# Optimization experiments

Measured on AMD Instinct MI355X. Metric: run time of the kernel, lower is better.

Reference implementation:

```python
import jax, jax.numpy as jnp
import numpy as np

N_NODES = 100000
N_EDGES = 1600000
N_FEAT = 128
N_HID = 128
N_CLS = 40
DROP_P = 0.5


def setup_inputs() -> dict:
    key = jax.random.key(0)
    k1, k2, k3, k4 = jax.random.split(key, 4)
    x = jax.random.normal(k1, (N_NODES, N_FEAT), dtype=jnp.float32)
    edge_index = jax.random.randint(k2, (2, N_EDGES), 0, N_NODES, dtype=jnp.int32)
    W1 = jax.random.normal(k3, (N_FEAT, N_HID), dtype=jnp.float32) / np.sqrt(N_FEAT)
    b1 = jnp.zeros((N_HID,), dtype=jnp.float32)
    W2 = jax.random.normal(k4, (N_HID, N_CLS), dtype=jnp.float32) / np.sqrt(N_HID)
    b2 = jnp.zeros((N_CLS,), dtype=jnp.float32)
    return {"x": x, "edge_index": edge_index, "W1": W1, "b1": b1, "W2": W2, "b2": b2}


def _gcn_norm(edge_index, num_nodes):
    # add self-loops, then symmetric normalization D^-1/2 (A+I) D^-1/2
    loops = jnp.arange(num_nodes, dtype=edge_index.dtype)
    src = jnp.concatenate([edge_index[0], loops])
    dst = jnp.concatenate([edge_index[1], loops])
    deg = jax.ops.segment_sum(jnp.ones_like(dst, dtype=jnp.float32), dst,
                              num_segments=num_nodes)
    deg_isqrt = jax.lax.rsqrt(deg)  # deg >= 1 thanks to self-loops
    norm = deg_isqrt[src] * deg_isqrt[dst]  # [E+N]
    return src, dst, norm


def _gcn_conv(x, src, dst, norm, W, b, num_nodes):
    h = x @ W                                   # [N, out]
    msg = h[src] * norm[:, None]                # gather + scale, [E+N, out]
    out = jax.ops.segment_sum(msg, dst, num_segments=num_nodes)  # scatter-add
    return out + b


def reference(x, edge_index, W1, b1, W2, b2):
    num_nodes = x.shape[0]
    src, dst, norm = _gcn_norm(edge_index, num_nodes)
    h = _gcn_conv(x, src, dst, norm, W1, b1, num_nodes)
    h = jax.nn.relu(h)
    # dropout(p=0.5, training=True) with a fixed key for determinism
    keep = jax.random.uniform(jax.random.key(42), h.shape) >= DROP_P
    h = jnp.where(keep, h / (1.0 - DROP_P), 0.0)
    out = _gcn_conv(h, src, dst, norm, W2, b2, num_nodes)
    return out
```

## Files before the change

kernel.cpp:

```cpp
#include <hip/hip_runtime.h>

#define N_NODES 100000
#define N_EDGES 1600000
#define NBUCK 196
#define G1B 1563
#define FB 391
#define FEDGE 4096
#define BCAP 9216

typedef __attribute__((ext_vector_type(8))) short short8v;
typedef __attribute__((ext_vector_type(4))) float f32x4;

__device__ __forceinline__ unsigned pack_bf16(float a, float b){
  unsigned ua = __float_as_uint(a), ub = __float_as_uint(b);
  ua = ua + 0x7fffu + ((ua >> 16) & 1u);
  ub = ub + 0x7fffu + ((ub >> 16) & 1u);
  return (ua >> 16) | (ub & 0xffff0000u);
}
__device__ __forceinline__ unsigned short bf16_of(float a){
  unsigned ua = __float_as_uint(a);
  ua = ua + 0x7fffu + ((ua >> 16) & 1u);
  return (unsigned short)(ua >> 16);
}
__device__ __forceinline__ float bf_lo(unsigned u){ return __uint_as_float(u << 16); }
__device__ __forceinline__ float bf_hi(unsigned u){ return __uint_as_float(u & 0xffff0000u); }

__device__ __forceinline__ unsigned tf_rotl(unsigned x, int r){ return (x<<r)|(x>>(32-r)); }

__device__ __forceinline__ unsigned dropout_keep(unsigned e){
  unsigned x0 = 0u, x1 = e;
  const unsigned k0 = 0u, k1v = 42u;
  const unsigned k2 = 0x1BD11BDAu ^ k0 ^ k1v;
#define TF_R(r) { x0 += x1; x1 = tf_rotl(x1,(r)); x1 ^= x0; }
  x0 += k0; x1 += k1v;
  TF_R(13) TF_R(15) TF_R(26) TF_R(6)
  x0 += k1v; x1 += k2 + 1u;
  TF_R(17) TF_R(29) TF_R(16) TF_R(24)
  x0 += k2; x1 += k0 + 2u;
  TF_R(13) TF_R(15) TF_R(26) TF_R(6)
  x0 += k0; x1 += k1v + 3u;
  TF_R(17) TF_R(29) TF_R(16) TF_R(24)
  x0 += k1v; x1 += k2 + 4u;
  TF_R(13) TF_R(15) TF_R(26) TF_R(6)
  x0 += k2; x1 += k0 + 5u;
#undef TF_R
  return (x0 ^ x1) >> 31;
}

__global__ void k_init(const float* __restrict__ W1, const float* __restrict__ W2,
                       unsigned short* __restrict__ W1T, unsigned short* __restrict__ W2T48,
                       int* __restrict__ bcur2){
  int b = blockIdx.x, t = threadIdx.x;
  if (b < 64){
    int idx = b*256 + t;
    int k = idx >> 7, n = idx & 127;
    W1T[n*128 + k] = bf16_of(W1[idx]);
  } else {
    if (t < NBUCK) bcur2[t] = 0;
    for (int i = t; i < 48*128; i += 256){
      int c = i >> 7, k = i & 127;
      W2T48[c*128 + k] = (c < 40) ? bf16_of(W2[k*40 + c]) : (unsigned short)0;
    }
  }
}

__launch_bounds__(256)
__global__ void k_B(const float* __restrict__ x, const unsigned short* __restrict__ W1T,
                    unsigned short* __restrict__ h1u,
                    const int* __restrict__ src, const int* __restrict__ dst,
                    int* __restrict__ bcur2, unsigned* __restrict__ tmp, int N, int E){
  __shared__ int hist[4][200];
  int t = threadIdx.x;
  if (blockIdx.x < FB){
    int fb = blockIdx.x;
    int w = t >> 6, lane = t & 63;
    for (int i = lane; i < NBUCK; i += 64) hist[w][i] = 0;
    __syncthreads();
    int e0 = fb*FEDGE;
    #pragma unroll 4
    for (int j = 0; j < FEDGE/256; j++){
      int e = e0 + t + j*256;
      if (e < E) atomicAdd(&hist[w][dst[e] >> 9], 1);
    }
    __syncthreads();
    if (t < NBUCK){
      int c0 = hist[0][t], c1 = hist[1][t], c2 = hist[2][t], c3 = hist[3][t];
      int tot = c0 + c1 + c2 + c3;
      int base = 0;
      if (tot > 0) base = t*BCAP + atomicAdd(&bcur2[t], tot);
      hist[0][t] = base;
      hist[1][t] = base + c0;
      hist[2][t] = base + c0 + c1;
      hist[3][t] = base + c0 + c1 + c2;
    }
    __syncthreads();
    #pragma unroll 4
    for (int j = 0; j < FEDGE/256; j++){
      int e = e0 + t + j*256;
      if (e < E){
        int d = dst[e], s = src[e];
        int p = atomicAdd(&hist[w][d >> 9], 1);
        tmp[p] = ((unsigned)(d & 511) << 17) | (unsigned)s;
      }
    }
    return;
  }
  int gb = blockIdx.x - FB;
  if (gb >= G1B) return;
  int w = t >> 6, l = t & 63;
  int lo = l & 15, hi = l >> 4;
  int rowA = gb*64 + w*16 + lo;
  int rA = (rowA < N) ? rowA : (N-1);
  const float4* xr = (const float4*)(x + (size_t)rA*128);

  short8v a[4];
  #pragma unroll
  for (int kk = 0; kk < 4; kk++){
    float4 f0 = xr[kk*8 + 2*hi];
    float4 f1 = xr[kk*8 + 2*hi + 1];
    union { short8v v; unsigned u[4]; } A;
    A.u[0] = pack_bf16(f0.x, f0.y);
    A.u[1] = pack_bf16(f0.z, f0.w);
    A.u[2] = pack_bf16(f1.x, f1.y);
    A.u[3] = pack_bf16(f1.z, f1.w);
    a[kk] = A.v;
  }
  int rowC0 = gb*64 + w*16 + hi*4;
  #pragma unroll
  for (int tt = 0; tt < 8; tt++){
    int n0 = tt*16;
    const uint4* brow = (const uint4*)(W1T + (n0 + lo)*128);
    f32x4 acc = {0.f, 0.f, 0.f, 0.f};
    #pragma unroll
    for (int kk = 0; kk < 4; kk++){
      union { short8v v; uint4 q; } B;
      B.q = brow[kk*4 + hi];
      acc = __builtin_amdgcn_mfma_f32_16x16x32_bf16(a[kk], B.v, acc, 0, 0, 0);
    }
    int colC = n0 + lo;
    #pragma unroll
    for (int r = 0; r < 4; r++){
      int rc = rowC0 + r;
      if (rc < N) h1u[(size_t)rc*128 + colC] = bf16_of(acc[r]);
    }
  }
}

__launch_bounds__(1024)
__global__ void k_hist(const unsigned* __restrict__ tmp, const int* __restrict__ bcur2,
                       int* __restrict__ degi, int* __restrict__ off,
                       float* __restrict__ dii, int N){
  __shared__ int cur[512];
  __shared__ int wtot[8];
  int b = blockIdx.x, t = threadIdx.x;
  if (t < 512) cur[t] = 0;
  __syncthreads();
  int m = bcur2[b];
  int base = b*BCAP;
  int node0 = b << 9;
  for (int i = t; i < m; i += 1024)
    atomicAdd(&cur[tmp[base + i] >> 17], 1);
  __syncthreads();
  if (t < 512){
    int v = cur[t];
    int lane = t & 63, w = t >> 6;
    int incl = v;
    for (int d = 1; d < 64; d <<= 1){
      int y = __shfl_up(incl, d);
      if (lane >= d) incl += y;
    }
    if (lane == 63) wtot[w] = incl;
    __syncthreads();
    int wb = 0;
    for (int i = 0; i < w; i++) wb += wtot[i];
    int excl = wb + incl - v;
    int n = node0 + t;
    if (n < N){
      degi[n] = v;
      off[n]  = base + excl;
      dii[n]  = rsqrtf((float)(v + 1));
    }
  }
}

__launch_bounds__(1024)
__global__ void k_csort(const unsigned* __restrict__ tmp, int2* __restrict__ csre,
                        const int* __restrict__ off, const int* __restrict__ bcur2,
                        const float* __restrict__ dii, int N){
  __shared__ int   cur[512];
  __shared__ float dl[512];
  int b = blockIdx.x, t = threadIdx.x;
  int node0 = b << 9;
  if (t < 512){
    int n = node0 + t;
    cur[t] = (n < N) ? off[n] : 0;
    dl[t]  = (n < N) ? dii[n] : 0.f;
  }
  __syncthreads();
  int m = bcur2[b];
  int base = b*BCAP;
  for (int i = t; i < m; i += 1024){
    unsigned e = tmp[base + i];
    int dloc = e >> 17;
    int s = e & 0x1FFFFu;
    float w = dii[s] * dl[dloc];
    int p = atomicAdd(&cur[dloc], 1);
    csre[p] = make_int2(s, __float_as_int(w));
  }
}

__launch_bounds__(256)
__global__ void k_agg1(const unsigned* __restrict__ h1g, unsigned* __restrict__ Bbg,
                       const int2* __restrict__ csre, const int* __restrict__ off,
                       const int* __restrict__ degi, const float* __restrict__ dii,
                       const float* __restrict__ b1, int N){
  int n = blockIdx.x*4 + (threadIdx.x >> 6);
  int lane = threadIdx.x & 63;
  if (n >= N) return;
  n = __builtin_amdgcn_readfirstlane(n);
  float din = dii[n];
  float s2 = din*din;
  unsigned su = h1g[(size_t)n*64 + lane];
  float a0 = bf_lo(su)*s2, a1 = bf_hi(su)*s2;
  int o = off[n], cnt = degi[n];
  int i = 0;
  for (; i + 8 <= cnt; i += 8){
    int2 e0 = csre[o+i+0], e1 = csre[o+i+1], e2 = csre[o+i+2], e3 = csre[o+i+3];
    int2 e4 = csre[o+i+4], e5 = csre[o+i+5], e6 = csre[o+i+6], e7 = csre[o+i+7];
    unsigned u0 = h1g[(size_t)e0.x*64 + lane];
    unsigned u1 = h1g[(size_t)e1.x*64 + lane];
    unsigned u2 = h1g[(size_t)e2.x*64 + lane];
    unsigned u3 = h1g[(size_t)e3.x*64 + lane];
    unsigned u4 = h1g[(size_t)e4.x*64 + lane];
    unsigned u5 = h1g[(size_t)e5.x*64 + lane];
    unsigned u6 = h1g[(size_t)e6.x*64 + lane];
    unsigned u7 = h1g[(size_t)e7.x*64 + lane];
    float w0 = __int_as_float(e0.y), w1 = __int_as_float(e1.y);
    float w2 = __int_as_float(e2.y), w3 = __int_as_float(e3.y);
    float w4 = __int_as_float(e4.y), w5 = __int_as_float(e5.y);
    float w6 = __int_as_float(e6.y), w7 = __int_as_float(e7.y);
    a0 = fmaf(bf_lo(u0), w0, a0); a1 = fmaf(bf_hi(u0), w0, a1);
    a0 = fmaf(bf_lo(u1), w1, a0); a1 = fmaf(bf_hi(u1), w1, a1);
    a0 = fmaf(bf_lo(u2), w2, a0); a1 = fmaf(bf_hi(u2), w2, a1);
    a0 = fmaf(bf_lo(u3), w3, a0); a1 = fmaf(bf_hi(u3), w3, a1);
    a0 = fmaf(bf_lo(u4), w4, a0); a1 = fmaf(bf_hi(u4), w4, a1);
    a0 = fmaf(bf_lo(u5), w5, a0); a1 = fmaf(bf_hi(u5), w5, a1);
    a0 = fmaf(bf_lo(u6), w6, a0); a1 = fmaf(bf_hi(u6), w6, a1);
    a0 = fmaf(bf_lo(u7), w7, a0); a1 = fmaf(bf_hi(u7), w7, a1);
  }
  for (; i < cnt; ++i){
    int2 e = csre[o+i];
    unsigned u = h1g[(size_t)e.x*64 + lane];
    float w = __int_as_float(e.y);
    a0 = fmaf(bf_lo(u), w, a0); a1 = fmaf(bf_hi(u), w, a1);
  }
  float2 bb = *(const float2*)(b1 + lane*2);
  a0 = fmaxf(a0 + bb.x, 0.f);
  a1 = fmaxf(a1 + bb.y, 0.f);
  unsigned e0i = (unsigned)n*128u + (unsigned)lane*2u;
  a0 = dropout_keep(e0i)      ? a0*2.f : 0.f;
  a1 = dropout_keep(e0i + 1u) ? a1*2.f : 0.f;
  Bbg[(size_t)n*64 + lane] = pack_bf16(a0, a1);
}

__launch_bounds__(256)
__global__ void k_gemm2(const unsigned* __restrict__ Bbg, const unsigned short* __restrict__ W2T48,
                        unsigned short* __restrict__ h2p, int N){
  int t = threadIdx.x;
  int w = t >> 6, l = t & 63;
  int lo = l & 15, hi = l >> 4;
  int rowA = blockIdx.x*64 + w*16 + lo;
  int rA = (rowA < N) ? rowA : (N-1);
  const uint4* ar = (const uint4*)(Bbg + (size_t)rA*64);

  short8v a[4];
  #pragma unroll
  for (int kk = 0; kk < 4; kk++){
    union { short8v v; uint4 q; } A;
    A.q = ar[kk*4 + hi];
    a[kk] = A.v;
  }
  int rowC0 = blockIdx.x*64 + w*16 + hi*4;
  #pragma unroll
  for (int tt = 0; tt < 3; tt++){
    int n0 = tt*16;
    const uint4* brow = (const uint4*)(W2T48 + (n0 + lo)*128);
    f32x4 acc = {0.f, 0.f, 0.f, 0.f};
    #pragma unroll
    for (int kk = 0; kk < 4; kk++){
      union { short8v v; uint4 q; } B;
      B.q = brow[kk*4 + hi];
      acc = __builtin_amdgcn_mfma_f32_16x16x32_bf16(a[kk], B.v, acc, 0, 0, 0);
    }
    int colC = n0 + lo;
    #pragma unroll
    for (int r = 0; r < 4; r++){
      int rc = rowC0 + r;
      if (rc < N) h2p[(size_t)rc*64 + colC] = bf16_of(acc[r]);
    }
  }
}

__launch_bounds__(256)
__global__ void k_agg2(const unsigned* __restrict__ h2p, float* __restrict__ out,
                       const int2* __restrict__ csre, const int* __restrict__ off,
                       const int* __restrict__ degi, const float* __restrict__ dii,
                       const float* __restrict__ b2, int N){
  int n = blockIdx.x*4 + (threadIdx.x >> 6);
  int lane31 = threadIdx.x & 31;
  int lane   = threadIdx.x & 63;
  if (n >= N) return;
  n = __builtin_amdgcn_readfirstlane(n);
  float din = dii[n];
  float sq = din*din;
  unsigned su = h2p[(size_t)n*32 + lane31];
  float a0 = bf_lo(su)*sq, a1 = bf_hi(su)*sq;
  int o = off[n], cnt = degi[n];
  int i = 0;
  for (; i + 8 <= cnt; i += 8){
    int2 e0 = csre[o+i+0], e1 = csre[o+i+1], e2 = csre[o+i+2], e3 = csre[o+i+3];
    int2 e4 = csre[o+i+4], e5 = csre[o+i+5], e6 = csre[o+i+6], e7 = csre[o+i+7];
    unsigned u0 = h2p[(size_t)e0.x*32 + lane31];
    unsigned u1 = h2p[(size_t)e1.x*32 + lane31];
    unsigned u2 = h2p[(size_t)e2.x*32 + lane31];
    unsigned u3 = h2p[(size_t)e3.x*32 + lane31];
    unsigned u4 = h2p[(size_t)e4.x*32 + lane31];
    unsigned u5 = h2p[(size_t)e5.x*32 + lane31];
    unsigned u6 = h2p[(size_t)e6.x*32 + lane31];
    unsigned u7 = h2p[(size_t)e7.x*32 + lane31];
    float w0 = __int_as_float(e0.y), w1 = __int_as_float(e1.y);
    float w2 = __int_as_float(e2.y), w3 = __int_as_float(e3.y);
    float w4 = __int_as_float(e4.y), w5 = __int_as_float(e5.y);
    float w6 = __int_as_float(e6.y), w7 = __int_as_float(e7.y);
    a0 = fmaf(bf_lo(u0), w0, a0); a1 = fmaf(bf_hi(u0), w0, a1);
    a0 = fmaf(bf_lo(u1), w1, a0); a1 = fmaf(bf_hi(u1), w1, a1);
    a0 = fmaf(bf_lo(u2), w2, a0); a1 = fmaf(bf_hi(u2), w2, a1);
    a0 = fmaf(bf_lo(u3), w3, a0); a1 = fmaf(bf_hi(u3), w3, a1);
    a0 = fmaf(bf_lo(u4), w4, a0); a1 = fmaf(bf_hi(u4), w4, a1);
    a0 = fmaf(bf_lo(u5), w5, a0); a1 = fmaf(bf_hi(u5), w5, a1);
    a0 = fmaf(bf_lo(u6), w6, a0); a1 = fmaf(bf_hi(u6), w6, a1);
    a0 = fmaf(bf_lo(u7), w7, a0); a1 = fmaf(bf_hi(u7), w7, a1);
  }
  for (; i < cnt; ++i){
    int2 e = csre[o+i];
    unsigned u = h2p[(size_t)e.x*32 + lane31];
    float w = __int_as_float(e.y);
    a0 = fmaf(bf_lo(u), w, a0); a1 = fmaf(bf_hi(u), w, a1);
  }
  if (lane < 20){
    float2 bb = *(const float2*)(b2 + lane*2);
    a0 += bb.x;
    a1 += bb.y;
    *(float2*)(out + (size_t)n*40 + lane*2) = make_float2(a0, a1);
  }
}

extern "C" void kernel_launch(void* const* d_in, const int* in_sizes, int n_in,
                              void* d_out, int out_size, void* d_ws, size_t ws_size,
                              hipStream_t stream){
  const float* x  = (const float*)d_in[0];
  const int*   ei = (const int*)  d_in[1];
  const float* W1 = (const float*)d_in[2];
  const float* b1 = (const float*)d_in[3];
  const float* W2 = (const float*)d_in[4];
  const float* b2 = (const float*)d_in[5];
  float* out = (float*)d_out;
  char* ws = (char*)d_ws;
  const int N = N_NODES, E = N_EDGES;
  const int* srcv = ei;
  const int* dstv = ei + E;

  int*   bcur2 = (int*)  (ws + 0);
  int*   off   = (int*)  (ws + 8192);
  int*   degi  = (int*)  (ws + 417792);
  float* dii   = (float*)(ws + 827392);
  unsigned short* W1T   = (unsigned short*)(ws + 1236992);
  unsigned short* W2T48 = (unsigned short*)(ws + 1269760);
  unsigned* tmp = (unsigned*)(ws + 1290240);
  int2*     csre= (int2*)   (ws + 8519680);
  unsigned short* h1u = (unsigned short*)(ws + 23068672);
  unsigned*       h1g = (unsigned*)      (ws + 23068672);
  unsigned short* h2p = (unsigned short*)(ws + 23068672);
  unsigned*       Bbg = (unsigned*)      (ws + 56623104);

  k_init<<<65, 256, 0, stream>>>(W1, W2, W1T, W2T48, bcur2);
  k_B<<<FB + G1B, 256, 0, stream>>>(x, W1T, h1u, srcv, dstv, bcur2, tmp, N, E);
  k_hist<<<NBUCK, 1024, 0, stream>>>(tmp, bcur2, degi, off, dii, N);
  k_csort<<<NBUCK, 1024, 0, stream>>>(tmp, csre, off, bcur2, dii, N);

  k_agg1 <<<N/4, 256, 0, stream>>>(h1g, Bbg, csre, off, degi, dii, b1, N);
  k_gemm2<<<(N + 63)/64, 256, 0, stream>>>(Bbg, W2T48, h2p, N);
  k_agg2 <<<N/4, 256, 0, stream>>>((const unsigned*)h2p, out, csre, off, degi, dii, b2, N);
}
```

Before: 210.6 us.

## Co-schedule GEMM1 blocks with histogram and CSR sort kernels to fill idle CUs

Restructures the preprocessing stage. Weight conversion and edge bucketing now run together in one kernel, and bcur2 is zeroed with a memset instead. The first GEMM is split across the histogram/prefix kernel and the CSR-sort kernel so its blocks fill the GPU alongside those 196-block kernels, which previously had few blocks. The hist and sort kernels drop from 1024 to 256 threads per block, so each thread handles more work, in exchange for sharing the machine with GEMM blocks.

```diff
diff --git a/kernel.cpp b/kernel.cpp
--- a/kernel.cpp
+++ b/kernel.cpp
@@ -4,6 +4,7 @@
 #define N_EDGES 1600000
 #define NBUCK 196
 #define G1B 1563
+#define GA1 950
 #define FB 391
 #define FEDGE 4096
 #define BCAP 9216
@@ -47,66 +48,10 @@
   return (x0 ^ x1) >> 31;
 }
 
-__global__ void k_init(const float* __restrict__ W1, const float* __restrict__ W2,
-                       unsigned short* __restrict__ W1T, unsigned short* __restrict__ W2T48,
-                       int* __restrict__ bcur2){
-  int b = blockIdx.x, t = threadIdx.x;
-  if (b < 64){
-    int idx = b*256 + t;
-    int k = idx >> 7, n = idx & 127;
-    W1T[n*128 + k] = bf16_of(W1[idx]);
-  } else {
-    if (t < NBUCK) bcur2[t] = 0;
-    for (int i = t; i < 48*128; i += 256){
-      int c = i >> 7, k = i & 127;
-      W2T48[c*128 + k] = (c < 40) ? bf16_of(W2[k*40 + c]) : (unsigned short)0;
-    }
-  }
-}
-
-__launch_bounds__(256)
-__global__ void k_B(const float* __restrict__ x, const unsigned short* __restrict__ W1T,
-                    unsigned short* __restrict__ h1u,
-                    const int* __restrict__ src, const int* __restrict__ dst,
-                    int* __restrict__ bcur2, unsigned* __restrict__ tmp, int N, int E){
-  __shared__ int hist[4][200];
-  int t = threadIdx.x;
-  if (blockIdx.x < FB){
-    int fb = blockIdx.x;
-    int w = t >> 6, lane = t & 63;
-    for (int i = lane; i < NBUCK; i += 64) hist[w][i] = 0;
-    __syncthreads();
-    int e0 = fb*FEDGE;
-    #pragma unroll 4
-    for (int j = 0; j < FEDGE/256; j++){
-      int e = e0 + t + j*256;
-      if (e < E) atomicAdd(&hist[w][dst[e] >> 9], 1);
-    }
-    __syncthreads();
-    if (t < NBUCK){
-      int c0 = hist[0][t], c1 = hist[1][t], c2 = hist[2][t], c3 = hist[3][t];
-      int tot = c0 + c1 + c2 + c3;
-      int base = 0;
-      if (tot > 0) base = t*BCAP + atomicAdd(&bcur2[t], tot);
-      hist[0][t] = base;
-      hist[1][t] = base + c0;
-      hist[2][t] = base + c0 + c1;
-      hist[3][t] = base + c0 + c1 + c2;
-    }
-    __syncthreads();
-    #pragma unroll 4
-    for (int j = 0; j < FEDGE/256; j++){
-      int e = e0 + t + j*256;
-      if (e < E){
-        int d = dst[e], s = src[e];
-        int p = atomicAdd(&hist[w][d >> 9], 1);
-        tmp[p] = ((unsigned)(d & 511) << 17) | (unsigned)s;
-      }
-    }
-    return;
-  }
-  int gb = blockIdx.x - FB;
-  if (gb >= G1B) return;
+__device__ __forceinline__ void gemm1_block(int gb, int t,
+                                            const float* __restrict__ x,
+                                            const unsigned short* __restrict__ W1T,
+                                            unsigned short* __restrict__ h1u, int N){
   int w = t >> 6, l = t & 63;
   int lo = l & 15, hi = l >> 4;
   int rowA = gb*64 + w*16 + lo;
@@ -146,25 +91,82 @@
   }
 }
 
-__launch_bounds__(1024)
-__global__ void k_hist(const unsigned* __restrict__ tmp, const int* __restrict__ bcur2,
-                       int* __restrict__ degi, int* __restrict__ off,
-                       float* __restrict__ dii, int N){
+__launch_bounds__(256)
+__global__ void k_p0(const float* __restrict__ W1, const float* __restrict__ W2,
+                     unsigned short* __restrict__ W1T, unsigned short* __restrict__ W2T48,
+                     const int* __restrict__ src, const int* __restrict__ dst,
+                     int* __restrict__ bcur2, unsigned* __restrict__ tmp, int E){
+  __shared__ int hist[4][200];
+  int t = threadIdx.x;
+  if (blockIdx.x < 64){
+    int idx = blockIdx.x*256 + t;
+    int k = idx >> 7, n = idx & 127;
+    W1T[n*128 + k] = bf16_of(W1[idx]);
+    return;
+  }
+  if (blockIdx.x == 64){
+    for (int i = t; i < 48*128; i += 256){
+      int c = i >> 7, k = i & 127;
+      W2T48[c*128 + k] = (c < 40) ? bf16_of(W2[k*40 + c]) : (unsigned short)0;
+    }
+    return;
+  }
+  int fb = blockIdx.x - 65;
+  int w = t >> 6, lane = t & 63;
+  for (int i = lane; i < NBUCK; i += 64) hist[w][i] = 0;
+  __syncthreads();
+  int e0 = fb*FEDGE;
+  #pragma unroll 4
+  for (int j = 0; j < FEDGE/256; j++){
+    int e = e0 + t + j*256;
+    if (e < E) atomicAdd(&hist[w][dst[e] >> 9], 1);
+  }
+  __syncthreads();
+  if (t < NBUCK){
+    int c0 = hist[0][t], c1 = hist[1][t], c2 = hist[2][t], c3 = hist[3][t];
+    int tot = c0 + c1 + c2 + c3;
+    int base = 0;
+    if (tot > 0) base = t*BCAP + atomicAdd(&bcur2[t], tot);
+    hist[0][t] = base;
+    hist[1][t] = base + c0;
+    hist[2][t] = base + c0 + c1;
+    hist[3][t] = base + c0 + c1 + c2;
+  }
+  __syncthreads();
+  #pragma unroll 4
+  for (int j = 0; j < FEDGE/256; j++){
+    int e = e0 + t + j*256;
+    if (e < E){
+      int d = dst[e], s = src[e];
+      int p = atomicAdd(&hist[w][d >> 9], 1);
+      tmp[p] = ((unsigned)(d & 511) << 17) | (unsigned)s;
+    }
+  }
+}
+
+__launch_bounds__(256)
+__global__ void k_p1(const float* __restrict__ x, const unsigned short* __restrict__ W1T,
+                     unsigned short* __restrict__ h1u,
+                     const unsigned* __restrict__ tmp, const int* __restrict__ bcur2,
+                     int* __restrict__ degi, int* __restrict__ off,
+                     float* __restrict__ dii, int N){
   __shared__ int cur[512];
-  __shared__ int wtot[8];
-  int b = blockIdx.x, t = threadIdx.x;
-  if (t < 512) cur[t] = 0;
-  __syncthreads();
-  int m = bcur2[b];
-  int base = b*BCAP;
-  int node0 = b << 9;
-  for (int i = t; i < m; i += 1024)
-    atomicAdd(&cur[tmp[base + i] >> 17], 1);
-  __syncthreads();
-  if (t < 512){
-    int v = cur[t];
+  __shared__ int wtot[4];
+  int t = threadIdx.x;
+  if (blockIdx.x < NBUCK){
+    int b = blockIdx.x;
+    cur[t] = 0; cur[t + 256] = 0;
+    __syncthreads();
+    int m = bcur2[b];
+    int base = b*BCAP;
+    int node0 = b << 9;
+    for (int i = t; i < m; i += 256)
+      atomicAdd(&cur[tmp[base + i] >> 17], 1);
+    __syncthreads();
+    int c0 = cur[2*t], c1 = cur[2*t + 1];
+    int s = c0 + c1;
     int lane = t & 63, w = t >> 6;
-    int incl = v;
+    int incl = s;
     for (int d = 1; d < 64; d <<= 1){
       int y = __shfl_up(incl, d);
       if (lane >= d) incl += y;
@@ -173,40 +175,56 @@
     __syncthreads();
     int wb = 0;
     for (int i = 0; i < w; i++) wb += wtot[i];
-    int excl = wb + incl - v;
-    int n = node0 + t;
-    if (n < N){
-      degi[n] = v;
-      off[n]  = base + excl;
-      dii[n]  = rsqrtf((float)(v + 1));
-    }
-  }
-}
-
-__launch_bounds__(1024)
-__global__ void k_csort(const unsigned* __restrict__ tmp, int2* __restrict__ csre,
-                        const int* __restrict__ off, const int* __restrict__ bcur2,
-                        const float* __restrict__ dii, int N){
+    int exclPair = wb + incl - s;
+    int n0 = node0 + 2*t, n1 = n0 + 1;
+    if (n0 < N){
+      degi[n0] = c0;
+      off[n0]  = base + exclPair;
+      dii[n0]  = rsqrtf((float)(c0 + 1));
+    }
+    if (n1 < N){
+      degi[n1] = c1;
+      off[n1]  = base + exclPair + c0;
+      dii[n1]  = rsqrtf((float)(c1 + 1));
+    }
+    return;
+  }
+  int gb = blockIdx.x - NBUCK;
+  if (gb < GA1) gemm1_block(gb, t, x, W1T, h1u, N);
+}
+
+__launch_bounds__(256)
+__global__ void k_p2(const float* __restrict__ x, const unsigned short* __restrict__ W1T,
+                     unsigned short* __restrict__ h1u,
+                     const unsigned* __restrict__ tmp, int2* __restrict__ csre,
+                     const int* __restrict__ off, const int* __restrict__ bcur2,
+                     const float* __restrict__ dii, int N){
   __shared__ int   cur[512];
   __shared__ float dl[512];
-  int b = blockIdx.x, t = threadIdx.x;
-  int node0 = b << 9;
-  if (t < 512){
-    int n = node0 + t;
-    cur[t] = (n < N) ? off[n] : 0;
-    dl[t]  = (n < N) ? dii[n] : 0.f;
-  }
-  __syncthreads();
-  int m = bcur2[b];
-  int base = b*BCAP;
-  for (int i = t; i < m; i += 1024){
-    unsigned e = tmp[base + i];
-    int dloc = e >> 17;
-    int s = e & 0x1FFFFu;
-    float w = dii[s] * dl[dloc];
-    int p = atomicAdd(&cur[dloc], 1);
-    csre[p] = make_int2(s, __float_as_int(w));
-  }
+  int t = threadIdx.x;
+  if (blockIdx.x < NBUCK){
+    int b = blockIdx.x;
+    int node0 = b << 9;
+    for (int i = t; i < 512; i += 256){
+      int n = node0 + i;
+      cur[i] = (n < N) ? off[n] : 0;
+      dl[i]  = (n < N) ? dii[n] : 0.f;
+    }
+    __syncthreads();
+    int m = bcur2[b];
+    int base = b*BCAP;
+    for (int i = t; i < m; i += 256){
+      unsigned e = tmp[base + i];
+      int dloc = e >> 17;
+      int s = e & 0x1FFFFu;
+      float w = dii[s] * dl[dloc];
+      int p = atomicAdd(&cur[dloc], 1);
+      csre[p] = make_int2(s, __float_as_int(w));
+    }
+    return;
+  }
+  int gb = GA1 + (blockIdx.x - NBUCK);
+  if (gb < G1B) gemm1_block(gb, t, x, W1T, h1u, N);
 }
 
 __launch_bounds__(256)
@@ -383,10 +401,11 @@
   unsigned short* h2p = (unsigned short*)(ws + 23068672);
   unsigned*       Bbg = (unsigned*)      (ws + 56623104);
 
-  k_init<<<65, 256, 0, stream>>>(W1, W2, W1T, W2T48, bcur2);
-  k_B<<<FB + G1B, 256, 0, stream>>>(x, W1T, h1u, srcv, dstv, bcur2, tmp, N, E);
-  k_hist<<<NBUCK, 1024, 0, stream>>>(tmp, bcur2, degi, off, dii, N);
-  k_csort<<<NBUCK, 1024, 0, stream>>>(tmp, csre, off, bcur2, dii, N);
+  hipMemsetAsync(bcur2, 0, 1024, stream);
+
+  k_p0<<<65 + FB, 256, 0, stream>>>(W1, W2, W1T, W2T48, srcv, dstv, bcur2, tmp, E);
+  k_p1<<<NBUCK + GA1, 256, 0, stream>>>(x, W1T, h1u, tmp, bcur2, degi, off, dii, N);
+  k_p2<<<NBUCK + (G1B - GA1), 256, 0, stream>>>(x, W1T, h1u, tmp, csre, off, bcur2, dii, N);
 
   k_agg1 <<<N/4, 256, 0, stream>>>(h1g, Bbg, csre, off, degi, dii, b1, N);
   k_gemm2<<<(N + 63)/64, 256, 0, stream>>>(Bbg, W2T48, h2p, N);
```

Measured after the change: 223.2 us. 6.0% more time.
